# Kernel tuning notes

Hardware: AMD Instinct MI355X
Metric: run time of the kernel (lower is better)

Reference implementation:

```python
import jax, jax.numpy as jnp
import numpy as np

INTERVALS = (1, 2, 4, 8)  # MTGRU update interval per hidden chunk


def _laplacian_hat(adj):
    # PyG ChebConv 'sym' norm, edge_weight=None (binarized), lambda_max=2:
    # L_hat = 2L/lmax - I = -D^-1/2 A D^-1/2 with zero diagonal.
    n = adj.shape[0]
    A = jnp.where(adj != 0, 1.0, 0.0) * (1.0 - jnp.eye(n, dtype=jnp.float32))
    deg = A.sum(axis=1)
    dinv = jnp.where(deg > 0, deg ** -0.5, 0.0)
    return -(dinv[:, None] * A * dinv[None, :])


def _cheb(x, L, W, b):
    # Chebyshev recurrence. x: [..., N, F]; W: [K, F, O]
    Tx0 = x
    out = jnp.einsum('...nf,fo->...no', Tx0, W[0])
    if W.shape[0] > 1:
        Tx1 = jnp.einsum('mn,...nf->...mf', L, x)
        out = out + jnp.einsum('...nf,fo->...no', Tx1, W[1])
        for k in range(2, W.shape[0]):
            Tx2 = 2.0 * jnp.einsum('mn,...nf->...mf', L, Tx1) - Tx0
            out = out + jnp.einsum('...nf,fo->...no', Tx2, W[k])
            Tx0, Tx1 = Tx1, Tx2
    return out + b


def _mtgru(x, h, idx, wi, wh, bi, bh):
    # multi-timescale GRU: hidden chunk k only updates when idx % INTERVALS[k]==0
    hid = h.shape[-1]
    xr, xz, xn = jnp.split(x @ wi + bi, 3, axis=-1)
    hr, hz, hc = jnp.split(h @ wh + bh, 3, axis=-1)
    r = jax.nn.sigmoid(xr + hr)
    z = jax.nn.sigmoid(xz + hz)
    n = jnp.tanh(xn + r * hc)
    h_new = (1.0 - z) * n + z * h
    mask = jnp.repeat((idx % jnp.asarray(INTERVALS)) == 0, hid // len(INTERVALS))
    return jnp.where(mask, h_new, h)


def _fuse(xg, xcg, afc, c2s_w, c2s_b, s2c_w, s2c_b):
    # cross-graph fusion; both updates use the pre-fusion tensors
    xg_new = xg + (jnp.einsum('sc,...cf->...sf', afc, xcg) @ c2s_w + c2s_b)
    xcg_new = xcg + (jnp.einsum('sc,...sf->...cf', afc, xg) @ s2c_w + s2c_b)
    return xg_new, xcg_new


def reference(x_hist, features, c_x_hist, c_features, adj_sta, adj_city, afc_s2c,
              conv_w, conv_b, c_conv_w, c_conv_b,
              gru_wi, gru_wh, gru_bi, gru_bh,
              c_gru_wi, c_gru_wh, c_gru_bi, c_gru_bh,
              fc_w, fc_b, c_fc_w, c_fc_b,
              c2s_w, c2s_b, s2c_w, s2c_b):
    B, T_h, Ns, Dout = x_hist.shape
    Nc = c_x_hist.shape[2]
    H = gru_wh.shape[0]
    L_s = _laplacian_hat(adj_sta)
    L_c = _laplacian_hat(adj_city)

    # ---- history phase: all inputs known ahead, batch GCN + fusion over time ----
    x_all = jnp.moveaxis(jnp.concatenate([x_hist[:, :T_h - 1], features[:, 1:T_h]], -1), 1, 0)   # [Th-1,B,Ns,Din]
    xc_all = jnp.moveaxis(jnp.concatenate([c_x_hist[:, :T_h - 1], c_features[:, 1:T_h]], -1), 1, 0)
    xg = jax.nn.sigmoid(_cheb(x_all, L_s, conv_w, conv_b))
    xcg = jax.nn.sigmoid(_cheb(xc_all, L_c, c_conv_w, c_conv_b))
    xg, xcg = _fuse(xg, xcg, afc_s2c, c2s_w, c2s_b, s2c_w, s2c_b)
    x_gru = jnp.concatenate([x_all, xg], -1)
    xc_gru = jnp.concatenate([xc_all, xcg], -1)

    hn = jnp.zeros((B, Ns, H), jnp.float32)
    hcn = jnp.zeros((B, Nc, H), jnp.float32)

    def hist_step(carry, xs):
        hn, hcn, idx = carry
        xg_t, xcg_t = xs
        hn = _mtgru(xg_t, hn, idx, gru_wi, gru_wh, gru_bi, gru_bh)
        hcn = _mtgru(xcg_t, hcn, idx, c_gru_wi, c_gru_wh, c_gru_bi, c_gru_bh)
        return (hn, hcn, idx + 1), None

    (hn, hcn, idx), _ = jax.lax.scan(hist_step, (hn, hcn, jnp.int32(1)), (x_gru, xc_gru))

    feats_p = jnp.moveaxis(features[:, T_h:], 1, 0)      # [Tp,B,Ns,Dm]
    c_feats_p = jnp.moveaxis(c_features[:, T_h:], 1, 0)

    def pred_step(carry, xs):
        hn, hcn, x_prev, xc_prev, idx = carry
        f, cf = xs
        x = jnp.concatenate([x_prev, f], -1)
        xc = jnp.concatenate([xc_prev, cf], -1)
        xg = jax.nn.sigmoid(_cheb(x, L_s, conv_w, conv_b))
        xcg = jax.nn.sigmoid(_cheb(xc, L_c, c_conv_w, c_conv_b))
        xg, xcg = _fuse(xg, xcg, afc_s2c, c2s_w, c2s_b, s2c_w, s2c_b)
        hn2 = _mtgru(jnp.concatenate([x, xg], -1), hn, idx, gru_wi, gru_wh, gru_bi, gru_bh)
        hcn2 = _mtgru(jnp.concatenate([xc, xcg], -1), hcn, idx, c_gru_wi, c_gru_wh, c_gru_bi, c_gru_bh)
        y = hn2 @ fc_w + fc_b
        yc = hcn2 @ c_fc_w + c_fc_b
        return (hn2, hcn2, y, yc, idx + 1), (y, yc)

    init = (hn, hcn, x_hist[:, T_h - 1], c_x_hist[:, T_h - 1], idx)
    _, (ys, ycs) = jax.lax.scan(pred_step, init, (feats_p, c_feats_p))
    return jnp.moveaxis(ys, 0, 1), jnp.moveaxis(ycs, 0, 1)  # [B,Tp,Ns,1], [B,Tp,Nc,1]


def setup_inputs():
    key = jax.random.key(0)
    ks = jax.random.split(key, 24)
    B, Ns, Nc, T_h, T_p = 8, 4096, 256, 8, 24
    Din, Dout, H, G, K = 28, 1, 64, 64, 2
    Dm, T, Dgru = Din - Dout, T_h + T_p, Din + 64

    def w(k, shape, fan_in):
        return (jax.random.normal(k, shape, jnp.float32) / np.sqrt(fan_in)).astype(jnp.float32)

    return {
        'x_hist': jax.random.normal(ks[0], (B, T_h, Ns, Dout), jnp.float32),
        'features': jax.random.normal(ks[1], (B, T, Ns, Dm), jnp.float32),
        'c_x_hist': jax.random.normal(ks[2], (B, T_h, Nc, Dout), jnp.float32),
        'c_features': jax.random.normal(ks[3], (B, T, Nc, Dm), jnp.float32),
        'adj_sta': (jax.random.uniform(ks[4], (Ns, Ns)) < 0.004).astype(jnp.float32),
        'adj_city': (jax.random.uniform(ks[5], (Nc, Nc)) < 0.1).astype(jnp.float32),
        'afc_s2c': (jax.random.uniform(ks[6], (Ns, Nc)) < (4.0 / Nc)).astype(jnp.float32),
        'conv_w': w(ks[7], (K, Din, G), Din),
        'conv_b': jnp.zeros((G,), jnp.float32),
        'c_conv_w': w(ks[8], (K, Din, G), Din),
        'c_conv_b': jnp.zeros((G,), jnp.float32),
        'gru_wi': w(ks[9], (Dgru, 3 * H), Dgru),
        'gru_wh': w(ks[10], (H, 3 * H), H),
        'gru_bi': jnp.zeros((3 * H,), jnp.float32),
        'gru_bh': jnp.zeros((3 * H,), jnp.float32),
        'c_gru_wi': w(ks[11], (Dgru, 3 * H), Dgru),
        'c_gru_wh': w(ks[12], (H, 3 * H), H),
        'c_gru_bi': jnp.zeros((3 * H,), jnp.float32),
        'c_gru_bh': jnp.zeros((3 * H,), jnp.float32),
        'fc_w': w(ks[13], (H, Dout), H),
        'fc_b': jnp.zeros((Dout,), jnp.float32),
        'c_fc_w': w(ks[14], (H, Dout), H),
        'c_fc_b': jnp.zeros((Dout,), jnp.float32),
        'c2s_w': w(ks[15], (G, G), G),
        'c2s_b': jnp.zeros((G,), jnp.float32),
        's2c_w': w(ks[16], (G, G), G),
        's2c_b': jnp.zeros((G,), jnp.float32),
    }
```

## Files before the change

kernel.cpp:

```cpp
#include <hip/hip_runtime.h>
#include <math.h>

typedef short bf16x8 __attribute__((ext_vector_type(8)));
typedef float f32x4 __attribute__((ext_vector_type(4)));

#define B 8
#define NS 4096
#define NC 256
#define TH 8
#define TP 24
#define T_ALL 32
#define DIN 28
#define DM 27
#define G 64
#define H 64
#define NG3 192
#define NSTEP 31

#define NTHR 256
#define NBLK_B 1024
#define SROWS 32
#define CROWS 2
#define NBLK_A 2048
#define AS 16
#define AR 17

#define XCW 224
#define KIT 7
#define NT 16
#define WFRAG (KIT*NT*64*8)
#define CVFRAG (2*4*64*8)

#define WS_ELL 64
#define WF_ELL 32
#define WFT_ELL 128

struct Params {
  const float *x_hist, *feat_s, *c_x_hist, *feat_c, *adj_s, *adj_c, *afc;
  const float *conv_w, *conv_b, *c_conv_w, *c_conv_b;
  const float *gru_wi, *gru_wh, *gru_bi, *gru_bh;
  const float *c_gru_wi, *c_gru_wh, *c_gru_bi, *c_gru_bh;
  const float *fc_w, *fc_b, *c_fc_w, *c_fc_b;
  const float *c2s_w, *c2s_b, *s2c_w, *s2c_b;
  int *deg_s, *ellc_s; float *ellv_s, *dinv_s;
  int *deg_c, *ellc_c; float *ellv_c, *dinv_c;
  int *degf, *ellf;
  int *degfT, *ellfT;
  float *xg_s, *xg_c, *xp_s, *xp_c;
  unsigned short *xsh, *xsl;
  unsigned short *xch, *xcl;
  unsigned short *wSh, *wSl, *wCh, *wCl;
  unsigned short *wcvSh, *wcvSl, *wcvCh, *wcvCl;
  float *aA_s, *aA_c;
  float *out;
};

__device__ __forceinline__ float sigm_(float x) { return 1.0f / (1.0f + expf(-x)); }

__device__ __forceinline__ unsigned short bf16rn(float f) {
  unsigned u = __float_as_uint(f);
  u += 0x7fffu + ((u >> 16) & 1u);
  return (unsigned short)(u >> 16);
}
__device__ __forceinline__ float bf16tof(unsigned short h) {
  return __uint_as_float(((unsigned)h) << 16);
}
__device__ __forceinline__ void split1(float f, unsigned short& hi, unsigned short& lo) {
  hi = bf16rn(f);
  lo = bf16rn(f - bf16tof(hi));
}

__device__ __forceinline__ int sidx(int i, int c) {
  return i * 64 + (c ^ ((i & 7) << 3));
}

__device__ float wcat_val(int k, int c, const float* wi, const float* wh,
                          const float* bi, const float* bh) {
  if (k < 92)  { return (c < 192) ? wi[k * NG3 + c] : 0.0f; }
  if (k < 156) {
    int kk = k - 92;
    if (c < 128) return wh[kk * NG3 + c];
    if (c < 192) return 0.0f;
    return wh[kk * NG3 + (c - 64)];
  }
  if (k == 156) {
    if (c < 128) return bi[c] + bh[c];
    if (c < 192) return bi[c];
    return bh[c - 64];
  }
  return 0.0f;
}

__device__ float wcat2_val(int k, int c, const float* wi, const float* wh,
                           const float* bi, const float* bh,
                           const float* wm, const float* bm) {
  if (k < 92) return wcat_val(k, c, wi, wh, bi, bh);
  if (k < 156) {
    int f = k - 92;
    float s = 0.0f;
    for (int g = 0; g < G; g++)
      s += wm[f * G + g] * wcat_val(28 + g, c, wi, wh, bi, bh);
    return s;
  }
  if (k < 220) return wcat_val(92 + (k - 156), c, wi, wh, bi, bh);
  if (k == 220) {
    float s = wcat_val(156, c, wi, wh, bi, bh);
    for (int g = 0; g < G; g++)
      s += bm[g] * wcat_val(28 + g, c, wi, wh, bi, bh);
    return s;
  }
  return 0.0f;
}

__device__ __forceinline__ float xval(const Params& p, int sta, int hist, int step,
                                      int b, int n, int f) {
  if (f == 0) {
    if (hist) return sta ? p.x_hist[((size_t)b * TH + step) * NS + n]
                         : p.c_x_hist[((size_t)b * TH + step) * NC + n];
    return sta ? p.xp_s[b * NS + n] : p.xp_c[b * NC + n];
  }
  int tf = step + 1;
  return sta ? p.feat_s[(((size_t)b * T_ALL + tf) * NS + n) * DM + (f - 1)]
             : p.feat_c[(((size_t)b * T_ALL + tf) * NC + n) * DM + (f - 1)];
}

__device__ void build_tables(const Params& p, int bid, int tid, int nblk) {
  const int lane = tid & 63;
  const int gw = bid * 4 + (tid >> 6);
  const int nw = nblk * 4;

  for (int r = gw; r < NS; r += nw) {
    int base = 0;
    for (int n0 = 0; n0 < NS; n0 += 64) {
      int n = n0 + lane;
      float v = p.adj_s[(size_t)r * NS + n];
      bool fl = (v != 0.0f) && (n != r);
      unsigned long long m = __ballot(fl);
      if (fl) {
        int pos = base + (int)__popcll(m & ((1ull << lane) - 1ull));
        if (pos < WS_ELL) p.ellc_s[r * WS_ELL + pos] = n;
      }
      base += (int)__popcll(m);
    }
    int deg = base < WS_ELL ? base : WS_ELL;
    for (int s = deg + lane; s < WS_ELL; s += 64) p.ellc_s[r * WS_ELL + s] = 0;
    if (lane == 0) {
      p.deg_s[r] = deg;
      p.dinv_s[r] = base > 0 ? 1.0f / sqrtf((float)base) : 0.0f;
    }
  }
  for (int r = gw; r < NS; r += nw) {
    int base = 0;
    for (int n0 = 0; n0 < NC; n0 += 64) {
      int n = n0 + lane;
      bool fl = p.afc[(size_t)r * NC + n] != 0.0f;
      unsigned long long m = __ballot(fl);
      if (fl) {
        int pos = base + (int)__popcll(m & ((1ull << lane) - 1ull));
        if (pos < WF_ELL) p.ellf[r * WF_ELL + pos] = n;
      }
      base += (int)__popcll(m);
    }
    int deg = base < WF_ELL ? base : WF_ELL;
    for (int s = deg + lane; s < WF_ELL; s += 64) p.ellf[r * WF_ELL + s] = 0;
    if (lane == 0) p.degf[r] = deg;
  }
  for (int r = gw; r < NC; r += nw) {
    int base = 0;
    for (int n0 = 0; n0 < NC; n0 += 64) {
      int n = n0 + lane;
      float v = p.adj_c[(size_t)r * NC + n];
      bool fl = (v != 0.0f) && (n != r);
      unsigned long long m = __ballot(fl);
      if (fl) {
        int pos = base + (int)__popcll(m & ((1ull << lane) - 1ull));
        if (pos < WS_ELL) p.ellc_c[r * WS_ELL + pos] = n;
      }
      base += (int)__popcll(m);
    }
    int deg = base < WS_ELL ? base : WS_ELL;
    for (int s = deg + lane; s < WS_ELL; s += 64) p.ellc_c[r * WS_ELL + s] = 0;
    if (lane == 0) {
      p.deg_c[r] = deg;
      p.dinv_c[r] = base > 0 ? 1.0f / sqrtf((float)base) : 0.0f;
    }
  }
  for (int r = gw; r < NC; r += nw) {
    int base = 0;
    for (int n0 = 0; n0 < NS; n0 += 64) {
      int n = n0 + lane;
      bool fl = p.afc[(size_t)n * NC + r] != 0.0f;
      unsigned long long m = __ballot(fl);
      if (fl) {
        int pos = base + (int)__popcll(m & ((1ull << lane) - 1ull));
        if (pos < WFT_ELL) p.ellfT[r * WFT_ELL + pos] = n;
      }
      base += (int)__popcll(m);
    }
    int deg = base < WFT_ELL ? base : WFT_ELL;
    for (int s = deg + lane; s < WFT_ELL; s += 64) p.ellfT[r * WFT_ELL + s] = 0;
    if (lane == 0) p.degfT[r] = deg;
  }

  const int gid = bid * NTHR + tid, ntot = nblk * NTHR;
  for (int i = gid; i < B * NS; i += ntot)
    p.xp_s[i] = p.x_hist[((size_t)(i / NS) * TH + (TH - 1)) * NS + (i % NS)];
  for (int i = gid; i < B * NC; i += ntot)
    p.xp_c[i] = p.c_x_hist[((size_t)(i / NC) * TH + (TH - 1)) * NC + (i % NC)];

  for (int u = gid; u < WFRAG; u += ntot) {
    int j = u & 7, l = (u >> 3) & 63, t = (u >> 9) & 15, q = u >> 13;
    int k = q * 32 + ((l >> 4) << 3) + j;
    int c = t * 16 + (l & 15);
    float ws = wcat2_val(k, c, p.gru_wi, p.gru_wh, p.gru_bi, p.gru_bh, p.c2s_w, p.c2s_b);
    unsigned short hh, ll;
    split1(ws, hh, ll);
    p.wSh[u] = hh; p.wSl[u] = ll;
    float wc = wcat2_val(k, c, p.c_gru_wi, p.c_gru_wh, p.c_gru_bi, p.c_gru_bh, p.s2c_w, p.s2c_b);
    split1(wc, hh, ll);
    p.wCh[u] = hh; p.wCl[u] = ll;
  }
  for (int u = gid; u < CVFRAG; u += ntot) {
    int j = u & 7, l = (u >> 3) & 63, t = (u >> 9) & 3, q = u >> 11;
    int k = q * 32 + ((l >> 4) << 3) + j;
    int c = t * 16 + (l & 15);
    float vs = (k < 56) ? p.conv_w[k * G + c] : 0.0f;
    unsigned short hh, ll;
    split1(vs, hh, ll);
    p.wcvSh[u] = hh; p.wcvSl[u] = ll;
    float vc = (k < 56) ? p.c_conv_w[k * G + c] : 0.0f;
    split1(vc, hh, ll);
    p.wcvCh[u] = hh; p.wcvCl[u] = ll;
  }
  for (int u = gid; u < B * NS * XCW; u += ntot) {
    p.xsh[u] = ((u % XCW) == 220) ? 0x3F80 : 0;
    p.xsl[u] = 0;
  }
  for (int u = gid; u < B * NC * XCW; u += ntot) {
    p.xch[u] = ((u % XCW) == 220) ? 0x3F80 : 0;
    p.xcl[u] = 0;
  }
}

__device__ void ellv_fill(const Params& p, int gid, int ntot) {
  for (int s = gid; s < NS * WS_ELL; s += ntot) {
    int r = s >> 6, k = s & (WS_ELL - 1);
    p.ellv_s[s] = (k < p.deg_s[r]) ? -p.dinv_s[r] * p.dinv_s[p.ellc_s[s]] : 0.0f;
  }
  for (int s = gid; s < NC * WS_ELL; s += ntot) {
    int r = s >> 6, k = s & (WS_ELL - 1);
    p.ellv_c[s] = (k < p.deg_c[r]) ? -p.dinv_c[r] * p.dinv_c[p.ellc_c[s]] : 0.0f;
  }
}

__global__ __launch_bounds__(NTHR) void precompA2_kernel(Params p) {
  __shared__ unsigned short lh[AR * 64];
  __shared__ unsigned short llo[AR * 64];
  const int bid = blockIdx.x & 2047;
  const int step = blockIdx.x >> 11;
  const int hist = (step < TH - 1) ? 1 : 0;
  const int tid = threadIdx.x;
  const int b = bid >> 8;

  for (int u = tid; u < AR * 8; u += NTHR) {
    lh[sidx(u >> 3, 56 + (u & 7))] = 0;
    llo[sidx(u >> 3, 56 + (u & 7))] = 0;
  }

  for (int q = tid; q < AR * DIN; q += NTHR) {
    int i = q / DIN, f = q % DIN;
    int sta = (i < AS);
    int n;
    const int* cc; const float* vv; int trip;
    if (sta) {
      n = (bid * AS + i) & 4095;
      cc = &p.ellc_s[n * WS_ELL]; vv = &p.ellv_s[n * WS_ELL];
      trip = (p.deg_s[n] + 7) & ~7;
    } else {
      n = bid & 255;
      cc = &p.ellc_c[n * WS_ELL]; vv = &p.ellv_c[n * WS_ELL];
      trip = (p.deg_c[n] + 7) & ~7;
    }
    float xv = 0.0f, acc = 0.0f;
    if (f == 0) {
      if (hist) {
        const float* bh = sta ? (p.x_hist + ((size_t)b * TH + step) * NS)
                              : (p.c_x_hist + ((size_t)b * TH + step) * NC);
        xv = bh[n];
        for (int e = 0; e < trip; e += 8) {
          float xv8[8];
#pragma unroll
          for (int u = 0; u < 8; u++) xv8[u] = bh[cc[e + u]];
#pragma unroll
          for (int u = 0; u < 8; u++) acc += vv[e + u] * xv8[u];
        }
      }
    } else {
      const float* bf = sta
        ? (p.feat_s + ((size_t)(b * T_ALL + step + 1) * NS) * DM + (f - 1))
        : (p.feat_c + ((size_t)(b * T_ALL + step + 1) * NC) * DM + (f - 1));
      xv = bf[(size_t)n * DM];
      for (int e = 0; e < trip; e += 8) {
        float xv8[8];
#pragma unroll
        for (int u = 0; u < 8; u++) xv8[u] = bf[(size_t)cc[e + u] * DM];
#pragma unroll
        for (int u = 0; u < 8; u++) acc += vv[e + u] * xv8[u];
      }
    }
    unsigned short hh, ll;
    split1(xv, hh, ll);
    lh[sidx(i, f)] = hh; llo[sidx(i, f)] = ll;
    split1(acc, hh, ll);
    lh[sidx(i, 28 + f)] = hh; llo[sidx(i, 28 + f)] = ll;
  }
  __syncthreads();

  const int l = tid & 63;
  const int wv = tid >> 6;
  f32x4 a1; f32x4 a2;
  a1[0] = 0.f; a1[1] = 0.f; a1[2] = 0.f; a1[3] = 0.f;
  a2[0] = 0.f; a2[1] = 0.f; a2[2] = 0.f; a2[3] = 0.f;
  const bf16x8* WVSh = (const bf16x8*)p.wcvSh;
  const bf16x8* WVSl = (const bf16x8*)p.wcvSl;
  const bf16x8* WVCh = (const bf16x8*)p.wcvCh;
  const bf16x8* WVCl = (const bf16x8*)p.wcvCl;
#pragma unroll
  for (int q = 0; q < 2; q++) {
    int kc = q * 32 + ((l >> 4) << 3);
    bf16x8 xh = *(const bf16x8*)&lh[sidx(l & 15, kc)];
    bf16x8 xl = *(const bf16x8*)&llo[sidx(l & 15, kc)];
    bf16x8 ch_, cl_;
    if ((l & 15) == 0) {
      ch_ = *(const bf16x8*)&lh[sidx(AS, kc)];
      cl_ = *(const bf16x8*)&llo[sidx(AS, kc)];
    } else {
#pragma unroll
      for (int j = 0; j < 8; j++) { ch_[j] = 0; cl_[j] = 0; }
    }
    int u = (q * 4 + wv) * 64 + l;
    bf16x8 bh_ = WVSh[u];
    bf16x8 bl_ = WVSl[u];
    a1 = __builtin_amdgcn_mfma_f32_16x16x32_bf16(xh, bh_, a1, 0, 0, 0);
    a1 = __builtin_amdgcn_mfma_f32_16x16x32_bf16(xl, bh_, a1, 0, 0, 0);
    a1 = __builtin_amdgcn_mfma_f32_16x16x32_bf16(xh, bl_, a1, 0, 0, 0);
    bf16x8 gh_ = WVCh[u];
    bf16x8 gl_ = WVCl[u];
    a2 = __builtin_amdgcn_mfma_f32_16x16x32_bf16(ch_, gh_, a2, 0, 0, 0);
    a2 = __builtin_amdgcn_mfma_f32_16x16x32_bf16(cl_, gh_, a2, 0, 0, 0);
    a2 = __builtin_amdgcn_mfma_f32_16x16x32_bf16(ch_, gl_, a2, 0, 0, 0);
  }

  const int g = wv * 16 + (l & 15);
  float* dst_s = p.aA_s + (size_t)step * (B * NS * G);
  float* dst_c = p.aA_c + (size_t)step * (B * NC * G);
  float bias = p.conv_b[g];
#pragma unroll
  for (int r = 0; r < 4; r++) {
    int row = ((l >> 4) << 2) + r;
    float v = a1[r] + bias;
    if (hist) v = sigm_(v);
    dst_s[(size_t)(bid * AS + row) * G + g] = v;
  }
  if ((l >> 4) == 0) {
    float v = a2[0] + p.c_conv_b[g];
    if (hist) v = sigm_(v);
    dst_c[(size_t)bid * G + g] = v;
  }
}

__global__ __launch_bounds__(NTHR) void stepA_lite_kernel(Params p, int step, int hist) {
  const int tid = threadIdx.x;
  const int l = tid & 63, wv = tid >> 6;
  const int wid = blockIdx.x * 4 + wv;
  if (wid < B * NS) {
    const int smn = wid, b = smn >> 12, n = smn & 4095;
    float x0 = hist ? p.x_hist[((size_t)b * TH + step) * NS + n] : p.xp_s[smn];
    float xg;
    const float* aA = p.aA_s + (size_t)step * (B * NS * G) + (size_t)smn * G;
    if (hist) {
      xg = aA[l];
    } else {
      float v = p.ellv_s[n * WS_ELL + l];
      int c = p.ellc_s[n * WS_ELL + l];
      float t = v * p.xp_s[b * NS + c];
#pragma unroll
      for (int m = 32; m; m >>= 1) t += __shfl_xor(t, m, 64);
      float acc = aA[l] + x0 * p.conv_w[l] + t * p.conv_w[DIN * G + l];
      xg = sigm_(acc);
      p.xg_s[(size_t)smn * G + l] = xg;
    }
    unsigned short hh, ll;
    split1(xg, hh, ll);
    size_t o = (size_t)smn * XCW;
    p.xsh[o + 28 + l] = hh; p.xsl[o + 28 + l] = ll;
    if (l < DIN) {
      float xv = (l == 0) ? x0
        : p.feat_s[(((size_t)b * T_ALL + step + 1) * NS + n) * DM + (l - 1)];
      split1(xv, hh, ll);
      p.xsh[o + l] = hh; p.xsl[o + l] = ll;
    }
  } else if (wid < B * NS + B * NC) {
    const int cm = wid - B * NS, b = cm >> 8, n = cm & 255;
    float x0 = hist ? p.c_x_hist[((size_t)b * TH + step) * NC + n] : p.xp_c[cm];
    float xg;
    const float* aA = p.aA_c + (size_t)step * (B * NC * G) + (size_t)cm * G;
    if (hist) {
      xg = aA[l];
    } else {
      float v = p.ellv_c[n * WS_ELL + l];
      int c = p.ellc_c[n * WS_ELL + l];
      float t = v * p.xp_c[b * NC + c];
#pragma unroll
      for (int m = 32; m; m >>= 1) t += __shfl_xor(t, m, 64);
      float acc = aA[l] + x0 * p.c_conv_w[l] + t * p.c_conv_w[DIN * G + l];
      xg = sigm_(acc);
      p.xg_c[(size_t)cm * G + l] = xg;
    }
    unsigned short hh, ll;
    split1(xg, hh, ll);
    size_t o = (size_t)cm * XCW;
    p.xch[o + 28 + l] = hh; p.xcl[o + 28 + l] = ll;
    if (l < DIN) {
      float xv = (l == 0) ? x0
        : p.feat_c[(((size_t)b * T_ALL + step + 1) * NC + n) * DM + (l - 1)];
      split1(xv, hh, ll);
      p.xch[o + l] = hh; p.xcl[o + l] = ll;
    }
  }
}

__global__ __launch_bounds__(NTHR) void stepA_kernel(Params p, int step, int hist) {
  __shared__ float xa[AR][DIN];
  __shared__ float lx[AR][DIN];
  const int bid = blockIdx.x, tid = threadIdx.x;
  for (int q = tid; q < AR * DIN; q += NTHR) {
    int i = q / DIN, f = q % DIN;
    int sta = (i < AS);
    int b, n;
    const int* cc; const float* vv; int trip;
    if (sta) {
      int smn = bid * AS + i; b = smn >> 12; n = smn & 4095;
      cc = &p.ellc_s[n * WS_ELL]; vv = &p.ellv_s[n * WS_ELL];
      trip = (p.deg_s[n] + 7) & ~7;
    } else {
      b = bid >> 8; n = bid & 255;
      cc = &p.ellc_c[n * WS_ELL]; vv = &p.ellv_c[n * WS_ELL];
      trip = (p.deg_c[n] + 7) & ~7;
    }
    float xv = xval(p, sta, hist, step, b, n, f);
    xa[i][f] = xv;
    unsigned short hh, ll;
    split1(xv, hh, ll);
    if (sta) {
      size_t o = (size_t)(bid * AS + i) * XCW + f;
      p.xsh[o] = hh; p.xsl[o] = ll;
    } else {
      size_t o = (size_t)bid * XCW + f;
      p.xch[o] = hh; p.xcl[o] = ll;
    }
    float acc = 0.0f;
    for (int e = 0; e < trip; e += 8) {
      float xv8[8];
#pragma unroll
      for (int u = 0; u < 8; u++) xv8[u] = xval(p, sta, hist, step, b, cc[e + u], f);
#pragma unroll
      for (int u = 0; u < 8; u++) acc += vv[e + u] * xv8[u];
    }
    lx[i][f] = acc;
  }
  __syncthreads();
  for (int q = tid; q < AR * G; q += NTHR) {
    int i = q >> 6, g = q & 63;
    int sta = (i < AS);
    const float* W = sta ? p.conv_w : p.c_conv_w;
    float acc = (sta ? p.conv_b : p.c_conv_b)[g];
#pragma unroll 4
    for (int f = 0; f < DIN; f++)
      acc += xa[i][f] * W[f * G + g] + lx[i][f] * W[DIN * G + f * G + g];
    float s = sigm_(acc);
    unsigned short hh, ll;
    split1(s, hh, ll);
    if (sta) {
      p.xg_s[(size_t)(bid * AS + i) * G + g] = s;
      size_t o = (size_t)(bid * AS + i) * XCW + 28 + g;
      p.xsh[o] = hh; p.xsl[o] = ll;
    } else {
      p.xg_c[(size_t)bid * G + g] = s;
      size_t o = (size_t)bid * XCW + 28 + g;
      p.xch[o] = hh; p.xcl[o] = ll;
    }
  }
}

__global__ __launch_bounds__(NTHR, 4) void stepB_kernel(Params p, int step, int hist, int idx) {
  __shared__ float cityfc[4][CROWS];
  __shared__ float fcs[4][SROWS];
  const int bid = blockIdx.x, tid = threadIdx.x;
  unsigned short* xsh = p.xsh + (size_t)bid * SROWS * XCW;
  unsigned short* xsl = p.xsl + (size_t)bid * SROWS * XCW;
  unsigned short* xch = p.xch + (size_t)bid * CROWS * XCW;
  unsigned short* xcl = p.xcl + (size_t)bid * CROWS * XCW;

#pragma unroll
  for (int k = 0; k < (SROWS * G) / NTHR; k++) {
    int q = tid + k * NTHR;
    int i = q >> 6, g = q & 63;
    int smn = bid * SROWS + i; int b = smn >> 12; int r = smn & 4095;
    int dg = p.degf[r];
    const int* cc = &p.ellf[r * WF_ELL];
    size_t bb = (size_t)b * NC;
    float acc = 0.0f;
    int e = 0;
    for (; e + 4 <= dg; e += 4) {
      acc += p.xg_c[(bb + cc[e]) * G + g] + p.xg_c[(bb + cc[e + 1]) * G + g]
           + p.xg_c[(bb + cc[e + 2]) * G + g] + p.xg_c[(bb + cc[e + 3]) * G + g];
    }
    for (; e < dg; e++) acc += p.xg_c[(bb + cc[e]) * G + g];
    unsigned short hh, ll;
    split1(acc, hh, ll);
    xsh[(size_t)i * XCW + 92 + g] = hh;
    xsl[(size_t)i * XCW + 92 + g] = ll;
  }
  {
    int g = (tid >> 2) & 63;
    int quar = tid & 3;
#pragma unroll
    for (int ci = 0; ci < CROWS; ci++) {
      int cm = bid * CROWS + ci; int b = cm >> 8; int r = cm & 255;
      int dg = p.degfT[r];
      const int* cc = &p.ellfT[r * WFT_ELL];
      int dq = (dg + 3) >> 2;
      int e0 = quar * dq;
      int e1 = e0 + dq; if (e1 > dg) e1 = dg; if (e0 > dg) e0 = dg;
      size_t bb = (size_t)b * NS;
      float acc = 0.0f;
      int e = e0;
      for (; e + 4 <= e1; e += 4) {
        acc += p.xg_s[(bb + cc[e]) * G + g] + p.xg_s[(bb + cc[e + 1]) * G + g]
             + p.xg_s[(bb + cc[e + 2]) * G + g] + p.xg_s[(bb + cc[e + 3]) * G + g];
      }
      for (; e < e1; e++) acc += p.xg_s[(bb + cc[e]) * G + g];
      acc += __shfl_down(acc, 2, 4);
      acc += __shfl_down(acc, 1, 4);
      if (quar == 0) {
        unsigned short hh, ll;
        split1(acc, hh, ll);
        xch[(size_t)ci * XCW + 92 + g] = hh;
        xcl[(size_t)ci * XCW + 92 + g] = ll;
      }
    }
  }
  __syncthreads();

  const int l = tid & 63;
  const int wv = tid >> 6;
  f32x4 accS[8];
  f32x4 accC[4];
#pragma unroll
  for (int t = 0; t < 8; t++) { accS[t][0] = 0.f; accS[t][1] = 0.f; accS[t][2] = 0.f; accS[t][3] = 0.f; }
#pragma unroll
  for (int t = 0; t < 4; t++) { accC[t][0] = 0.f; accC[t][1] = 0.f; accC[t][2] = 0.f; accC[t][3] = 0.f; }
  const bf16x8* WSh = (const bf16x8*)p.wSh;
  const bf16x8* WSl = (const bf16x8*)p.wSl;
  const bf16x8* WCh = (const bf16x8*)p.wCh;
  const bf16x8* WCl = (const bf16x8*)p.wCl;

  for (int q = 0; q < KIT; q++) {
    int kc = q * 32 + ((l >> 4) << 3);
    bf16x8 aS0h = *(const bf16x8*)(xsh + (size_t)(l & 15) * XCW + kc);
    bf16x8 aS0l = *(const bf16x8*)(xsl + (size_t)(l & 15) * XCW + kc);
    bf16x8 aS1h = *(const bf16x8*)(xsh + (size_t)(16 + (l & 15)) * XCW + kc);
    bf16x8 aS1l = *(const bf16x8*)(xsl + (size_t)(16 + (l & 15)) * XCW + kc);
    bf16x8 aCh, aCl;
    if ((l & 15) < CROWS) {
      aCh = *(const bf16x8*)(xch + (size_t)(l & 15) * XCW + kc);
      aCl = *(const bf16x8*)(xcl + (size_t)(l & 15) * XCW + kc);
    } else {
#pragma unroll
      for (int j = 0; j < 8; j++) { aCh[j] = 0; aCl[j] = 0; }
    }
    int base = q * (NT * 64) + l;
#pragma unroll
    for (int tt = 0; tt < 4; tt++) {
      int toff = base + (wv + tt * 4) * 64;
      bf16x8 wh_ = WSh[toff];
      bf16x8 wl_ = WSl[toff];
      accS[tt]     = __builtin_amdgcn_mfma_f32_16x16x32_bf16(aS0h, wh_, accS[tt], 0, 0, 0);
      accS[tt]     = __builtin_amdgcn_mfma_f32_16x16x32_bf16(aS0l, wh_, accS[tt], 0, 0, 0);
      accS[tt]     = __builtin_amdgcn_mfma_f32_16x16x32_bf16(aS0h, wl_, accS[tt], 0, 0, 0);
      accS[4 + tt] = __builtin_amdgcn_mfma_f32_16x16x32_bf16(aS1h, wh_, accS[4 + tt], 0, 0, 0);
      accS[4 + tt] = __builtin_amdgcn_mfma_f32_16x16x32_bf16(aS1l, wh_, accS[4 + tt], 0, 0, 0);
      accS[4 + tt] = __builtin_amdgcn_mfma_f32_16x16x32_bf16(aS1h, wl_, accS[4 + tt], 0, 0, 0);
      bf16x8 ch_ = WCh[toff];
      bf16x8 cl_ = WCl[toff];
      accC[tt] = __builtin_amdgcn_mfma_f32_16x16x32_bf16(aCh, ch_, accC[tt], 0, 0, 0);
      accC[tt] = __builtin_amdgcn_mfma_f32_16x16x32_bf16(aCl, ch_, accC[tt], 0, 0, 0);
      accC[tt] = __builtin_amdgcn_mfma_f32_16x16x32_bf16(aCh, cl_, accC[tt], 0, 0, 0);
    }
  }
  __syncthreads();

  const int pred = !hist;
  const int t_out = step - (TH - 1);
  const int j = wv * 16 + (l & 15);
  const int upd = ((idx & ((1 << wv) - 1)) == 0);
  float fcacc[8];
  {
    float fwj = p.fc_w[j];
#pragma unroll
    for (int rt = 0; rt < 2; rt++) {
#pragma unroll
      for (int r = 0; r < 4; r++) {
        int row = rt * 16 + ((l >> 4) << 2) + r;
        float rr = sigm_(accS[rt * 4 + 0][r]);
        float zz = sigm_(accS[rt * 4 + 1][r]);
        float nn = tanhf(accS[rt * 4 + 2][r] + rr * accS[rt * 4 + 3][r]);
        size_t o = (size_t)row * XCW + 156 + j;
        float ho = bf16tof(xsh[o]) + bf16tof(xsl[o]);
        float hn = upd ? ((1.0f - zz) * nn + zz * ho) : ho;
        unsigned short hh, ll;
        split1(hn, hh, ll);
        xsh[o] = hh; xsl[o] = ll;
        fcacc[rt * 4 + r] = fwj * hn;
      }
    }
  }
  float cfc[CROWS] = {0.f, 0.f};
  if ((l >> 4) == 0) {
    float fwj = p.c_fc_w[j];
#pragma unroll
    for (int r = 0; r < CROWS; r++) {
      float rr = sigm_(accC[0][r]);
      float zz = sigm_(accC[1][r]);
      float nn = tanhf(accC[2][r] + rr * accC[3][r]);
      size_t o = (size_t)r * XCW + 156 + j;
      float ho = bf16tof(xch[o]) + bf16tof(xcl[o]);
      float hn = upd ? ((1.0f - zz) * nn + zz * ho) : ho;
      unsigned short hh, ll;
      split1(hn, hh, ll);
      xch[o] = hh; xcl[o] = ll;
      cfc[r] = fwj * hn;
    }
  }
  if (pred) {
#pragma unroll
    for (int rt = 0; rt < 2; rt++) {
#pragma unroll
      for (int r = 0; r < 4; r++) {
        float v = fcacc[rt * 4 + r];
        v += __shfl_down(v, 8, 16);
        v += __shfl_down(v, 4, 16);
        v += __shfl_down(v, 2, 16);
        v += __shfl_down(v, 1, 16);
        if ((l & 15) == 0) fcs[wv][rt * 16 + ((l >> 4) << 2) + r] = v;
      }
    }
#pragma unroll
    for (int r = 0; r < CROWS; r++) {
      float v = cfc[r];
      v += __shfl_down(v, 8, 16);
      v += __shfl_down(v, 4, 16);
      v += __shfl_down(v, 2, 16);
      v += __shfl_down(v, 1, 16);
      if (l == 0) cityfc[wv][r] = v;
    }
    __syncthreads();
    if (tid < SROWS) {
      float y = fcs[0][tid] + fcs[1][tid] + fcs[2][tid] + fcs[3][tid] + p.fc_b[0];
      int smn = bid * SROWS + tid; int b = smn >> 12; int n = smn & 4095;
      p.out[((size_t)b * TP + t_out) * NS + n] = y;
      p.xp_s[smn] = y;
    }
    if (tid >= 64 && tid < 64 + CROWS) {
      int r = tid - 64;
      float y = cityfc[0][r] + cityfc[1][r] + cityfc[2][r] + cityfc[3][r] + p.c_fc_b[0];
      int cm = bid * CROWS + r; int b = cm >> 8; int n = cm & 255;
      p.out[(size_t)B * TP * NS + ((size_t)b * TP + t_out) * NC + n] = y;
      p.xp_c[cm] = y;
    }
  }
}

__global__ __launch_bounds__(NTHR) void build_kernel(Params p) {
  build_tables(p, blockIdx.x, threadIdx.x, gridDim.x);
}
__global__ __launch_bounds__(NTHR) void ellv_kernel(Params p) {
  ellv_fill(p, blockIdx.x * NTHR + threadIdx.x, gridDim.x * NTHR);
}

extern "C" void kernel_launch(void* const* d_in, const int* in_sizes, int n_in,
                              void* d_out, int out_size, void* d_ws, size_t ws_size,
                              hipStream_t stream) {
  Params p;
  p.x_hist   = (const float*)d_in[0];
  p.feat_s   = (const float*)d_in[1];
  p.c_x_hist = (const float*)d_in[2];
  p.feat_c   = (const float*)d_in[3];
  p.adj_s    = (const float*)d_in[4];
  p.adj_c    = (const float*)d_in[5];
  p.afc      = (const float*)d_in[6];
  p.conv_w   = (const float*)d_in[7];
  p.conv_b   = (const float*)d_in[8];
  p.c_conv_w = (const float*)d_in[9];
  p.c_conv_b = (const float*)d_in[10];
  p.gru_wi   = (const float*)d_in[11];
  p.gru_wh   = (const float*)d_in[12];
  p.gru_bi   = (const float*)d_in[13];
  p.gru_bh   = (const float*)d_in[14];
  p.c_gru_wi = (const float*)d_in[15];
  p.c_gru_wh = (const float*)d_in[16];
  p.c_gru_bi = (const float*)d_in[17];
  p.c_gru_bh = (const float*)d_in[18];
  p.fc_w     = (const float*)d_in[19];
  p.fc_b     = (const float*)d_in[20];
  p.c_fc_w   = (const float*)d_in[21];
  p.c_fc_b   = (const float*)d_in[22];
  p.c2s_w    = (const float*)d_in[23];
  p.c2s_b    = (const float*)d_in[24];
  p.s2c_w    = (const float*)d_in[25];
  p.s2c_b    = (const float*)d_in[26];

  char* wp = (char*)d_ws;
  auto alloc = [&](size_t bytes) -> char* {
    char* q = wp;
    wp += (bytes + 255) & ~(size_t)255;
    return q;
  };
  p.deg_s  = (int*)alloc(NS * 4);
  p.dinv_s = (float*)alloc(NS * 4);
  p.ellc_s = (int*)alloc((size_t)NS * WS_ELL * 4);
  p.ellv_s = (float*)alloc((size_t)NS * WS_ELL * 4);
  p.deg_c  = (int*)alloc(NC * 4);
  p.dinv_c = (float*)alloc(NC * 4);
  p.ellc_c = (int*)alloc((size_t)NC * WS_ELL * 4);
  p.ellv_c = (float*)alloc((size_t)NC * WS_ELL * 4);
  p.degf   = (int*)alloc(NS * 4);
  p.ellf   = (int*)alloc((size_t)NS * WF_ELL * 4);
  p.degfT  = (int*)alloc(NC * 4);
  p.ellfT  = (int*)alloc((size_t)NC * WFT_ELL * 4);
  p.xg_s   = (float*)alloc((size_t)B * NS * G * 4);
  p.xg_c   = (float*)alloc((size_t)B * NC * G * 4);
  p.xp_s   = (float*)alloc((size_t)B * NS * 4);
  p.xp_c   = (float*)alloc((size_t)B * NC * 4);
  p.xsh    = (unsigned short*)alloc((size_t)B * NS * XCW * 2);
  p.xsl    = (unsigned short*)alloc((size_t)B * NS * XCW * 2);
  p.xch    = (unsigned short*)alloc((size_t)B * NC * XCW * 2);
  p.xcl    = (unsigned short*)alloc((size_t)B * NC * XCW * 2);
  p.wSh    = (unsigned short*)alloc((size_t)WFRAG * 2);
  p.wSl    = (unsigned short*)alloc((size_t)WFRAG * 2);
  p.wCh    = (unsigned short*)alloc((size_t)WFRAG * 2);
  p.wCl    = (unsigned short*)alloc((size_t)WFRAG * 2);
  p.wcvSh  = (unsigned short*)alloc((size_t)CVFRAG * 2);
  p.wcvSl  = (unsigned short*)alloc((size_t)CVFRAG * 2);
  p.wcvCh  = (unsigned short*)alloc((size_t)CVFRAG * 2);
  p.wcvCl  = (unsigned short*)alloc((size_t)CVFRAG * 2);
  p.aA_s   = (float*)alloc((size_t)NSTEP * B * NS * G * 4);
  p.aA_c   = (float*)alloc((size_t)NSTEP * B * NC * G * 4);
  p.out    = (float*)d_out;

  const bool big = ((size_t)(wp - (char*)d_ws) <= ws_size);

  build_kernel<<<2048, NTHR, 0, stream>>>(p);
  ellv_kernel<<<2048, NTHR, 0, stream>>>(p);
  if (big) {
    precompA2_kernel<<<NSTEP * 2048, NTHR, 0, stream>>>(p);
    for (int step = 0; step < NSTEP; step++) {
      int hist = (step < TH - 1) ? 1 : 0;
      stepA_lite_kernel<<<(B * NS + B * NC) / 4, NTHR, 0, stream>>>(p, step, hist);
      Params pb = p;
      if (hist) {
        pb.xg_s = p.aA_s + (size_t)step * (B * NS * G);
        pb.xg_c = p.aA_c + (size_t)step * (B * NC * G);
      }
      stepB_kernel<<<NBLK_B, NTHR, 0, stream>>>(pb, step, hist, step + 1);
    }
  } else {
    for (int step = 0; step < NSTEP; step++) {
      int hist = (step < TH - 1) ? 1 : 0;
      stepA_kernel<<<NBLK_A, NTHR, 0, stream>>>(p, step, hist);
      stepB_kernel<<<NBLK_B, NTHR, 0, stream>>>(p, step, hist, step + 1);
    }
  }
}
```

Measured before the change: 2.930 ms.

## Fold next history step's input staging into stepB and widen ELL gather

For history steps 1..6, the per-step stepA_lite launch is skipped. The preceding stepB instead writes the next step's bf16 hi/lo input rows (x_hist, features and the precomputed conv activation) straight into the xsh/xch buffers, which removes a kernel launch and a global round trip per history step. The ELL gather in stepA is also rewritten to process 16 neighbours per iteration using vectorized int4/float4 index and weight loads. That requires the ELL rows to be padded to a multiple of 16, which may not hold for WS_ELL and could read past the stored neighbour data.

```diff
diff --git a/kernel.cpp b/kernel.cpp
--- a/kernel.cpp
+++ b/kernel.cpp
@@ -74,6 +74,34 @@
   return i * 64 + (c ^ ((i & 7) << 3));
 }
 
+__device__ __forceinline__ float gather16(const float* base, size_t stride,
+                                          const int* cc, const float* vv, int trip) {
+  float acc = 0.0f;
+  for (int e = 0; e < trip; e += 16) {
+    int4 c0 = *(const int4*)&cc[e];
+    int4 c1 = *(const int4*)&cc[e + 4];
+    int4 c2 = *(const int4*)&cc[e + 8];
+    int4 c3 = *(const int4*)&cc[e + 12];
+    float4 v0 = *(const float4*)&vv[e];
+    float4 v1 = *(const float4*)&vv[e + 4];
+    float4 v2 = *(const float4*)&vv[e + 8];
+    float4 v3 = *(const float4*)&vv[e + 12];
+    float x0 = base[(size_t)c0.x * stride], x1 = base[(size_t)c0.y * stride];
+    float x2 = base[(size_t)c0.z * stride], x3 = base[(size_t)c0.w * stride];
+    float x4 = base[(size_t)c1.x * stride], x5 = base[(size_t)c1.y * stride];
+    float x6 = base[(size_t)c1.z * stride], x7 = base[(size_t)c1.w * stride];
+    float x8 = base[(size_t)c2.x * stride], x9 = base[(size_t)c2.y * stride];
+    float xa = base[(size_t)c2.z * stride], xb = base[(size_t)c2.w * stride];
+    float xc = base[(size_t)c3.x * stride], xd = base[(size_t)c3.y * stride];
+    float xe = base[(size_t)c3.z * stride], xf = base[(size_t)c3.w * stride];
+    acc += v0.x * x0 + v0.y * x1 + v0.z * x2 + v0.w * x3
+         + v1.x * x4 + v1.y * x5 + v1.z * x6 + v1.w * x7
+         + v2.x * x8 + v2.y * x9 + v2.z * xa + v2.w * xb
+         + v3.x * xc + v3.y * xd + v3.z * xe + v3.w * xf;
+  }
+  return acc;
+}
+
 __device__ float wcat_val(int k, int c, const float* wi, const float* wh,
                           const float* bi, const float* bh) {
   if (k < 92)  { return (c < 192) ? wi[k * NG3 + c] : 0.0f; }
@@ -275,11 +303,11 @@
     if (sta) {
       n = (bid * AS + i) & 4095;
       cc = &p.ellc_s[n * WS_ELL]; vv = &p.ellv_s[n * WS_ELL];
-      trip = (p.deg_s[n] + 7) & ~7;
+      trip = (p.deg_s[n] + 15) & ~15;
     } else {
       n = bid & 255;
       cc = &p.ellc_c[n * WS_ELL]; vv = &p.ellv_c[n * WS_ELL];
-      trip = (p.deg_c[n] + 7) & ~7;
+      trip = (p.deg_c[n] + 15) & ~15;
     }
     float xv = 0.0f, acc = 0.0f;
     if (f == 0) {
@@ -287,26 +315,14 @@
         const float* bh = sta ? (p.x_hist + ((size_t)b * TH + step) * NS)
                               : (p.c_x_hist + ((size_t)b * TH + step) * NC);
         xv = bh[n];
-        for (int e = 0; e < trip; e += 8) {
-          float xv8[8];
-#pragma unroll
-          for (int u = 0; u < 8; u++) xv8[u] = bh[cc[e + u]];
-#pragma unroll
-          for (int u = 0; u < 8; u++) acc += vv[e + u] * xv8[u];
-        }
+        acc = gather16(bh, 1, cc, vv, trip);
       }
     } else {
       const float* bf = sta
         ? (p.feat_s + ((size_t)(b * T_ALL + step + 1) * NS) * DM + (f - 1))
         : (p.feat_c + ((size_t)(b * T_ALL + step + 1) * NC) * DM + (f - 1));
       xv = bf[(size_t)n * DM];
-      for (int e = 0; e < trip; e += 8) {
-        float xv8[8];
-#pragma unroll
-        for (int u = 0; u < 8; u++) xv8[u] = bf[(size_t)cc[e + u] * DM];
-#pragma unroll
-        for (int u = 0; u < 8; u++) acc += vv[e + u] * xv8[u];
-      }
+      acc = gather16(bf, DM, cc, vv, trip);
     }
     unsigned short hh, ll;
     split1(xv, hh, ll);
@@ -493,7 +509,8 @@
   }
 }
 
-__global__ __launch_bounds__(NTHR, 4) void stepB_kernel(Params p, int step, int hist, int idx) {
+__global__ __launch_bounds__(NTHR, 4) void stepB_kernel(Params p, int step, int hist,
+                                                        int idx, int fold) {
   __shared__ float cityfc[4][CROWS];
   __shared__ float fcs[4][SROWS];
   const int bid = blockIdx.x, tid = threadIdx.x;
@@ -678,6 +695,34 @@
       int cm = bid * CROWS + r; int b = cm >> 8; int n = cm & 255;
       p.out[(size_t)B * TP * NS + ((size_t)b * TP + t_out) * NC + n] = y;
       p.xp_c[cm] = y;
+    }
+  }
+  if (fold) {
+    const float* aAn_s = p.aA_s + (size_t)(step + 1) * (B * NS * G);
+    const float* aAn_c = p.aA_c + (size_t)(step + 1) * (B * NC * G);
+    for (int u = tid; u < SROWS * 92; u += NTHR) {
+      int i = u / 92, c = u % 92;
+      int smn = bid * SROWS + i; int b = smn >> 12; int n = smn & 4095;
+      float v;
+      if (c == 0)      v = p.x_hist[((size_t)b * TH + step + 1) * NS + n];
+      else if (c < 28) v = p.feat_s[(((size_t)b * T_ALL + step + 2) * NS + n) * DM + (c - 1)];
+      else             v = aAn_s[(size_t)smn * G + (c - 28)];
+      unsigned short hh, ll;
+      split1(v, hh, ll);
+      xsh[(size_t)i * XCW + c] = hh;
+      xsl[(size_t)i * XCW + c] = ll;
+    }
+    for (int u = tid; u < CROWS * 92; u += NTHR) {
+      int i = u / 92, c = u % 92;
+      int cm = bid * CROWS + i; int b = cm >> 8; int n = cm & 255;
+      float v;
+      if (c == 0)      v = p.c_x_hist[((size_t)b * TH + step + 1) * NC + n];
+      else if (c < 28) v = p.feat_c[(((size_t)b * T_ALL + step + 2) * NC + n) * DM + (c - 1)];
+      else             v = aAn_c[(size_t)cm * G + (c - 28)];
+      unsigned short hh, ll;
+      split1(v, hh, ll);
+      xch[(size_t)i * XCW + c] = hh;
+      xcl[(size_t)i * XCW + c] = ll;
     }
   }
 }
@@ -767,19 +812,22 @@
     precompA2_kernel<<<NSTEP * 2048, NTHR, 0, stream>>>(p);
     for (int step = 0; step < NSTEP; step++) {
       int hist = (step < TH - 1) ? 1 : 0;
-      stepA_lite_kernel<<<(B * NS + B * NC) / 4, NTHR, 0, stream>>>(p, step, hist);
+      bool skipA = (step >= 1 && step <= TH - 2);
+      if (!skipA)
+        stepA_lite_kernel<<<(B * NS + B * NC) / 4, NTHR, 0, stream>>>(p, step, hist);
       Params pb = p;
       if (hist) {
         pb.xg_s = p.aA_s + (size_t)step * (B * NS * G);
         pb.xg_c = p.aA_c + (size_t)step * (B * NC * G);
       }
-      stepB_kernel<<<NBLK_B, NTHR, 0, stream>>>(pb, step, hist, step + 1);
+      int fold = (hist && step + 1 <= TH - 2) ? 1 : 0;
+      stepB_kernel<<<NBLK_B, NTHR, 0, stream>>>(pb, step, hist, step + 1, fold);
     }
   } else {
     for (int step = 0; step < NSTEP; step++) {
       int hist = (step < TH - 1) ? 1 : 0;
       stepA_kernel<<<NBLK_A, NTHR, 0, stream>>>(p, step, hist);
-      stepB_kernel<<<NBLK_B, NTHR, 0, stream>>>(p, step, hist, step + 1);
-    }
-  }
-}
+      stepB_kernel<<<NBLK_B, NTHR, 0, stream>>>(p, step, hist, step + 1, 0);
+    }
+  }
+}
```

Measured after the change: 3.029 ms. 3.4% more time.
